# Performance work log

Measured on AMD Instinct MI355X. Metric: run time of the kernel, lower is better.

## Reference

```python
import jax, jax.numpy as jnp
import numpy as np

IN, HID, OUT = 128, 128, 128
NU, NI = 100000, 50000
E = 500000
NEG_SLOPE = 0.01  # torch F.leaky_relu default


def graph_conv(x_src, W, b, src, dst, n_dst):
    """DGL GraphConv with norm='right': sum messages into dst, divide by in-degree, add bias."""
    h = x_src @ W                                   # [n_src, d_out] -- apply weight first
    agg = jax.ops.segment_sum(h[src], dst, num_segments=n_dst)  # irregular gather + scatter-add
    deg = jax.ops.segment_sum(jnp.ones(dst.shape, h.dtype), dst, num_segments=n_dst)
    return agg / jnp.clip(deg, 1.0)[:, None] + b


def setup_inputs() -> dict:
    key = jax.random.key(0)
    ks = jax.random.split(key, 16)
    inp = {
        "x_user": jax.random.normal(ks[0], (NU, IN), jnp.float32),
        "x_item": jax.random.normal(ks[1], (NI, IN), jnp.float32),
        "src_rates": jax.random.randint(ks[2], (E,), 0, NU),
        "dst_rates": jax.random.randint(ks[3], (E,), 0, NI),
        "src_rev": jax.random.randint(ks[4], (E,), 0, NI),
        "dst_rev": jax.random.randint(ks[5], (E,), 0, NU),
        # layer 1 per-relation GraphConv params
        "W1_rates": jax.random.normal(ks[6], (IN, HID), jnp.float32) / np.sqrt(IN),
        "b1_rates": jnp.zeros((HID,), jnp.float32),
        "W1_rev": jax.random.normal(ks[7], (IN, HID), jnp.float32) / np.sqrt(IN),
        "b1_rev": jnp.zeros((HID,), jnp.float32),
        # layer 2 per-relation GraphConv params
        "W2_rates": jax.random.normal(ks[8], (HID, OUT), jnp.float32) / np.sqrt(HID),
        "b2_rates": jnp.zeros((OUT,), jnp.float32),
        "W2_rev": jax.random.normal(ks[9], (HID, OUT), jnp.float32) / np.sqrt(HID),
        "b2_rev": jnp.zeros((OUT,), jnp.float32),
    }
    return inp


def reference(x_user, x_item, src_rates, dst_rates, src_rev, dst_rev,
              W1_rates, b1_rates, W1_rev, b1_rev,
              W2_rates, b2_rates, W2_rev, b2_rev):
    # layer 1: HeteroGraphConv(sum) -- each dst type receives from its one incoming relation
    h_item = graph_conv(x_user, W1_rates, b1_rates, src_rates, dst_rates, NI)
    h_user = graph_conv(x_item, W1_rev, b1_rev, src_rev, dst_rev, NU)
    h_item = jax.nn.leaky_relu(h_item, NEG_SLOPE)
    h_user = jax.nn.leaky_relu(h_user, NEG_SLOPE)
    # layer 2
    o_item = graph_conv(h_user, W2_rates, b2_rates, src_rates, dst_rates, NI)
    o_user = graph_conv(h_item, W2_rev, b2_rev, src_rev, dst_rev, NU)
    return (o_user, o_item)
```

## Files before the change

### kernel.cpp

```cpp
#include <hip/hip_runtime.h>
#include <cstdint>
#include <cstddef>

#define NUSER 100000
#define NITEM 50000
#define NTOT  150000
#define NEDGE 500000
#define NEG_SLOPE 0.01f
#define PADW 136

#define BROWS 512
#define BSHIFT 9
#define NBUCK ((NTOT + BROWS - 1) / BROWS)
#define GCAP  8192
#define EPB   2048
#define NBINB ((NEDGE + EPB - 1) / EPB)
#define NENT  (2 * EPB)

typedef __attribute__((ext_vector_type(8))) short bf16x8;
typedef __attribute__((ext_vector_type(4))) float f32x4;

__device__ __forceinline__ unsigned short f2bf(float f) {
    unsigned int u = __builtin_bit_cast(unsigned int, f);
    unsigned int r = u + 0x7fffu + ((u >> 16) & 1u);
    return (unsigned short)(r >> 16);
}
__device__ __forceinline__ float bf2f(unsigned int b) {
    unsigned int u = (b & 0xffffu) << 16;
    return __builtin_bit_cast(float, u);
}
__device__ __forceinline__ unsigned int pack2(float lo, float hi) {
    return (unsigned int)f2bf(lo) | ((unsigned int)f2bf(hi) << 16);
}


__global__ __launch_bounds__(512) void bin_edges(const int* __restrict__ src_rates, const int* __restrict__ dst_rates,
                                                 const int* __restrict__ src_rev,   const int* __restrict__ dst_rev,
                                                 int* __restrict__ bcnt, unsigned int* __restrict__ bbuf) {
    __shared__ int h[NBUCK];
    __shared__ int hs[NBUCK];
    __shared__ int hbase[NBUCK];
    __shared__ int hcur[NBUCK];
    __shared__ int bsc[512];
    __shared__ unsigned int stage[NENT];

    int t = threadIdx.x;
    int e0 = blockIdx.x * EPB;
    int n = NEDGE - e0; if (n > EPB) n = EPB;

    for (int i = t; i < NBUCK; i += 512) h[i] = 0;
    __syncthreads();

    for (int i = t; i < n; i += 512) {
        int e = e0 + i;
        atomicAdd(&h[dst_rates[e] >> BSHIFT], 1);
        atomicAdd(&h[(NITEM + dst_rev[e]) >> BSHIFT], 1);
    }
    __syncthreads();

    int v = (t < NBUCK) ? h[t] : 0;
    bsc[t] = v;
    __syncthreads();
    for (int off = 1; off < 512; off <<= 1) {
        int x = (t >= off) ? bsc[t - off] : 0;
        __syncthreads();
        bsc[t] += x;
        __syncthreads();
    }
    if (t < NBUCK) {
        int run = bsc[t] - v;
        hs[t] = run;
        hcur[t] = run;
        hbase[t] = (v > 0) ? atomicAdd(&bcnt[t], v) : 0;
    }
    __syncthreads();

    for (int i = t; i < n; i += 512) {
        int e = e0 + i;
        int r1 = dst_rates[e];
        int p1 = atomicAdd(&hcur[r1 >> BSHIFT], 1);
        if (p1 < NENT)
            stage[p1] = ((unsigned)(r1 & (BROWS - 1)) << 17) | (unsigned)src_rates[e];
        int r2 = NITEM + dst_rev[e];
        int p2 = atomicAdd(&hcur[r2 >> BSHIFT], 1);
        if (p2 < NENT)
            stage[p2] = ((unsigned)(r2 & (BROWS - 1)) << 17) | (unsigned)src_rev[e];
    }
    __syncthreads();

    int wid = t >> 6, lane = t & 63;
    for (int b = wid; b < NBUCK; b += 8) {
        int cnt = h[b];
        if (cnt > NENT) cnt = NENT;
        int gb = hbase[b];
        int sb = hs[b];
        for (int i = lane; i < cnt; i += 64) {
            int gpos = gb + i;
            if (gpos < GCAP) bbuf[(size_t)b * GCAP + gpos] = stage[sb + i];
        }
    }
}


__global__ __launch_bounds__(256) void build_csr(const int* __restrict__ bcnt,
                                                 const unsigned int* __restrict__ bbuf,
                                                 int* __restrict__ rp, int* __restrict__ csr) {
    __shared__ unsigned int ent[GCAP];
    __shared__ int h[BROWS], hs[BROWS];
    __shared__ int bsc[256];

    int bk = blockIdx.x, t = threadIdx.x;

    int ps = 0;
    for (int i = t; i < bk; i += 256) ps += bcnt[i];
    bsc[t] = ps;
    __syncthreads();
    for (int off = 128; off > 0; off >>= 1) {
        if (t < off) bsc[t] += bsc[t + off];
        __syncthreads();
    }
    int base = bsc[0];
    int n = bcnt[bk];
    if (n > GCAP) n = GCAP;
    __syncthreads();

    const unsigned int* src = bbuf + (size_t)bk * GCAP;
    for (int i = t; i < n; i += 256) ent[i] = src[i];
    h[t] = 0; h[t + 256] = 0;
    __syncthreads();

    for (int i = t; i < n; i += 256) atomicAdd(&h[ent[i] >> 17], 1);
    __syncthreads();

    int v0 = h[2 * t], v1 = h[2 * t + 1];
    int ls = v0 + v1;
    bsc[t] = ls;
    __syncthreads();
    for (int off = 1; off < 256; off <<= 1) {
        int x = (t >= off) ? bsc[t - off] : 0;
        __syncthreads();
        bsc[t] += x;
        __syncthreads();
    }
    int run = bsc[t] - ls;
    hs[2 * t] = run;
    hs[2 * t + 1] = run + v0;
    __syncthreads();

    for (int r = t; r < BROWS; r += 256) {
        int row = bk * BROWS + r;
        if (row < NTOT) rp[row] = base + hs[r];
        h[r] = 0;
    }
    if (bk == 0 && t == 0) rp[NTOT] = 2 * NEDGE;
    __syncthreads();

    for (int i = t; i < n; i += 256) {
        unsigned int ev = ent[i];
        int rl = (int)(ev >> 17);
        int pos = base + hs[rl] + atomicAdd(&h[rl], 1);
        csr[pos] = (int)(ev & 0x1FFFFu);
    }
}


__global__ void wprep(const float* __restrict__ w0, const float* __restrict__ w1,
                      const float* __restrict__ w2, const float* __restrict__ w3,
                      unsigned short* __restrict__ wt) {
    const float* src = (blockIdx.x == 0) ? w0 : (blockIdx.x == 1) ? w1 : (blockIdx.x == 2) ? w2 : w3;
    unsigned short* dst = wt + (size_t)blockIdx.x * 128 * PADW;
    for (int i = threadIdx.x; i < 16384; i += 256) {
        int k = i >> 7, c = i & 127;
        dst[c * PADW + k] = f2bf(src[i]);
    }
}


__global__ __launch_bounds__(256) void aggregate_ep(const unsigned short* __restrict__ featA,
                                                    const unsigned short* __restrict__ featB,
                                                    const int* __restrict__ rp, const int* __restrict__ csr,
                                                    const float* __restrict__ bI, const float* __restrict__ bU,
                                                    unsigned short* __restrict__ outb,
                                                    float* __restrict__ outI, float* __restrict__ outU) {
    int row = blockIdx.x * 8 + (threadIdx.x >> 5);
    if (row >= NTOT) return;
    bool item = row < NITEM;
    const unsigned short* feat = item ? featA : featB;
    int l = threadIdx.x & 31;
    int sub = l >> 4, l16 = l & 15;
    int b = rp[row], e = rp[row + 1];
    float a0 = 0.f, a1 = 0.f, a2 = 0.f, a3 = 0.f, a4 = 0.f, a5 = 0.f, a6 = 0.f, a7 = 0.f;
    int j = b + sub;
    for (; j + 2 < e; j += 4) {
        int s0 = csr[j];
        int s1 = csr[j + 2];
        uint4 v0 = *((const uint4*)(feat + (size_t)s0 * 128) + l16);
        uint4 v1 = *((const uint4*)(feat + (size_t)s1 * 128) + l16);
        a0 += bf2f(v0.x); a1 += bf2f(v0.x >> 16);
        a2 += bf2f(v0.y); a3 += bf2f(v0.y >> 16);
        a4 += bf2f(v0.z); a5 += bf2f(v0.z >> 16);
        a6 += bf2f(v0.w); a7 += bf2f(v0.w >> 16);
        a0 += bf2f(v1.x); a1 += bf2f(v1.x >> 16);
        a2 += bf2f(v1.y); a3 += bf2f(v1.y >> 16);
        a4 += bf2f(v1.z); a5 += bf2f(v1.z >> 16);
        a6 += bf2f(v1.w); a7 += bf2f(v1.w >> 16);
    }
    if (j < e) {
        int s0 = csr[j];
        uint4 v0 = *((const uint4*)(feat + (size_t)s0 * 128) + l16);
        a0 += bf2f(v0.x); a1 += bf2f(v0.x >> 16);
        a2 += bf2f(v0.y); a3 += bf2f(v0.y >> 16);
        a4 += bf2f(v0.z); a5 += bf2f(v0.z >> 16);
        a6 += bf2f(v0.w); a7 += bf2f(v0.w >> 16);
    }
    a0 += __shfl_xor(a0, 16); a1 += __shfl_xor(a1, 16);
    a2 += __shfl_xor(a2, 16); a3 += __shfl_xor(a3, 16);
    a4 += __shfl_xor(a4, 16); a5 += __shfl_xor(a5, 16);
    a6 += __shfl_xor(a6, 16); a7 += __shfl_xor(a7, 16);
    if (sub == 0) {
        int deg = e - b;
        float inv = 1.0f / (float)(deg > 0 ? deg : 1);
        const float* bias = item ? bI : bU;
        float4 bv0 = ((const float4*)bias)[l16 * 2];
        float4 bv1 = ((const float4*)bias)[l16 * 2 + 1];
        float r0 = a0 * inv + bv0.x, r1 = a1 * inv + bv0.y;
        float r2 = a2 * inv + bv0.z, r3 = a3 * inv + bv0.w;
        float r4 = a4 * inv + bv1.x, r5 = a5 * inv + bv1.y;
        float r6 = a6 * inv + bv1.z, r7 = a7 * inv + bv1.w;
        if (outI) {
            float* o = item ? (outI + (size_t)row * 128) : (outU + (size_t)(row - NITEM) * 128);
            float4 o0, o1;
            o0.x = r0; o0.y = r1; o0.z = r2; o0.w = r3;
            o1.x = r4; o1.y = r5; o1.z = r6; o1.w = r7;
            ((float4*)o)[l16 * 2]     = o0;
            ((float4*)o)[l16 * 2 + 1] = o1;
        } else {
            r0 = r0 > 0.f ? r0 : NEG_SLOPE * r0;
            r1 = r1 > 0.f ? r1 : NEG_SLOPE * r1;
            r2 = r2 > 0.f ? r2 : NEG_SLOPE * r2;
            r3 = r3 > 0.f ? r3 : NEG_SLOPE * r3;
            r4 = r4 > 0.f ? r4 : NEG_SLOPE * r4;
            r5 = r5 > 0.f ? r5 : NEG_SLOPE * r5;
            r6 = r6 > 0.f ? r6 : NEG_SLOPE * r6;
            r7 = r7 > 0.f ? r7 : NEG_SLOPE * r7;
            uint4 o;
            o.x = pack2(r0, r1);
            o.y = pack2(r2, r3);
            o.z = pack2(r4, r5);
            o.w = pack2(r6, r7);
            *((uint4*)(outb + (size_t)row * 128) + l16) = o;
        }
    }
}


__global__ __launch_bounds__(256) void gemm_both(const float* __restrict__ xfU, const float* __restrict__ xfI,
                                                 const unsigned short* __restrict__ inB,
                                                 const unsigned short* __restrict__ wt0,
                                                 const unsigned short* __restrict__ wt1,
                                                 unsigned short* __restrict__ outB,
                                                 int nR0, int g0, int g1) {
    __shared__ __attribute__((aligned(16))) unsigned short wl[128 * PADW];
    __shared__ __attribute__((aligned(16))) unsigned short xl[64 * PADW];
    int t = threadIdx.x;
    int bi = blockIdx.x;
    bool reg0 = bi < g0;
    int tbeg = reg0 ? bi : bi - g0;
    int gstr = reg0 ? g0 : g1;
    int rbeg = reg0 ? 0 : nR0;
    int rcnt = reg0 ? nR0 : NTOT - nR0;
    int Nend = rbeg + rcnt;
    int nT = (rcnt + 63) / 64;
    const unsigned short* wt = reg0 ? wt0 : wt1;

    for (int i = t; i < 128 * PADW / 8; i += 256)
        ((uint4*)wl)[i] = ((const uint4*)wt)[i];

    int lane = t & 63, w = t >> 6;
    int l16 = lane & 15, kq = lane >> 4;
    int rowb = w * 16;

    for (int tt = tbeg; tt < nT; tt += gstr) {
        int row0 = rbeg + tt * 64;

        __syncthreads();
        if (xfU) {
            for (int i = t; i < 1024; i += 256) {
                int r = i >> 4, c = i & 15;
                int row = row0 + r;
                uint4 v = make_uint4(0u, 0u, 0u, 0u);
                if (row < Nend) {
                    const float* s = (row < NUSER) ? (xfU + (size_t)row * 128 + c * 8)
                                                   : (xfI + (size_t)(row - NUSER) * 128 + c * 8);
                    float4 a = ((const float4*)s)[0];
                    float4 b = ((const float4*)s)[1];
                    v.x = pack2(a.x, a.y);
                    v.y = pack2(a.z, a.w);
                    v.z = pack2(b.x, b.y);
                    v.w = pack2(b.z, b.w);
                }
                ((uint4*)xl)[r * (PADW / 8) + c] = v;
            }
        } else {
            for (int i = t; i < 1024; i += 256) {
                int r = i >> 4, c = i & 15;
                int row = row0 + r;
                uint4 v = make_uint4(0u, 0u, 0u, 0u);
                if (row < Nend) v = ((const uint4*)(inB + (size_t)row * 128))[c];
                ((uint4*)xl)[r * (PADW / 8) + c] = v;
            }
        }
        __syncthreads();

        f32x4 acc[8];
        #pragma unroll
        for (int i = 0; i < 8; ++i) acc[i] = (f32x4){0.f, 0.f, 0.f, 0.f};

        #pragma unroll
        for (int ks = 0; ks < 4; ++ks) {
            int ko = ks * 32 + kq * 8;
            bf16x8 af = *(const bf16x8*)&xl[(rowb + l16) * PADW + ko];
            #pragma unroll
            for (int t8 = 0; t8 < 8; ++t8) {
                bf16x8 bf = *(const bf16x8*)&wl[(t8 * 16 + l16) * PADW + ko];
                acc[t8] = __builtin_amdgcn_mfma_f32_16x16x32_bf16(af, bf, acc[t8], 0, 0, 0);
            }
        }

        #pragma unroll
        for (int t8 = 0; t8 < 8; ++t8) {
            #pragma unroll
            for (int j = 0; j < 4; ++j)
                xl[(rowb + kq * 4 + j) * PADW + t8 * 16 + l16] = f2bf(acc[t8][j]);
        }
        __syncthreads();
        for (int i = t; i < 1024; i += 256) {
            int r = i >> 4, c = i & 15;
            int row = row0 + r;
            if (row < Nend)
                ((uint4*)(outB + (size_t)row * 128))[c] = ((uint4*)xl)[r * (PADW / 8) + c];
        }
    }
}


extern "C" void kernel_launch(void* const* d_in, const int* in_sizes, int n_in,
                              void* d_out, int out_size, void* d_ws, size_t ws_size,
                              hipStream_t stream) {
    const float* x_user    = (const float*)d_in[0];
    const float* x_item    = (const float*)d_in[1];
    const int*   src_rates = (const int*)d_in[2];
    const int*   dst_rates = (const int*)d_in[3];
    const int*   src_rev   = (const int*)d_in[4];
    const int*   dst_rev   = (const int*)d_in[5];
    const float* W1_rates  = (const float*)d_in[6];
    const float* b1_rates  = (const float*)d_in[7];
    const float* W1_rev    = (const float*)d_in[8];
    const float* b1_rev    = (const float*)d_in[9];
    const float* W2_rates  = (const float*)d_in[10];
    const float* b2_rates  = (const float*)d_in[11];
    const float* W2_rev    = (const float*)d_in[12];
    const float* b2_rev    = (const float*)d_in[13];

    float* out    = (float*)d_out;
    float* o_user = out;
    float* o_item = out + (size_t)NUSER * 128;

    char* ws = (char*)d_ws;
    size_t off = 0;
    auto carve = [&](size_t bytes) -> void* {
        void* p = ws + off;
        off = (off + bytes + 255) & ~(size_t)255;
        return p;
    };
    unsigned short* A = (unsigned short*)carve((size_t)NTOT * 128 * 2);
    unsigned short* B = (unsigned short*)carve((size_t)NTOT * 128 * 2);
    int* rp    = (int*)carve((size_t)(NTOT + 1) * 4);
    int* bcnt  = (int*)carve((size_t)NBUCK * 4);
    int* csr   = (int*)carve((size_t)(2 * NEDGE) * 4);
    unsigned short* wtAll = (unsigned short*)carve((size_t)4 * 128 * PADW * 2);
    unsigned short* Wt1_rates = wtAll;
    unsigned short* Wt1_rev   = wtAll + 1 * (size_t)128 * PADW;
    unsigned short* Wt2_rates = wtAll + 2 * (size_t)128 * PADW;
    unsigned short* Wt2_rev   = wtAll + 3 * (size_t)128 * PADW;

    unsigned int* bbuf = (unsigned int*)B;

    hipMemsetAsync(bcnt, 0, (size_t)NBUCK * 4, stream);
    wprep<<<4, 256, 0, stream>>>(W1_rates, W1_rev, W2_rates, W2_rev, wtAll);
    bin_edges<<<NBINB, 512, 0, stream>>>(src_rates, dst_rates, src_rev, dst_rev, bcnt, bbuf);
    build_csr<<<NBUCK, 256, 0, stream>>>(bcnt, bbuf, rp, csr);

    int nbAgg = (NTOT + 7) / 8;

    gemm_both<<<528, 256, 0, stream>>>(x_user, x_item, nullptr,
                                       Wt1_rates, Wt1_rev, A, NUSER, 352, 176);
    aggregate_ep<<<nbAgg, 256, 0, stream>>>(A, A + (size_t)NUSER * 128, rp, csr,
                                            b1_rates, b1_rev, B, nullptr, nullptr);

    gemm_both<<<528, 256, 0, stream>>>(nullptr, nullptr, B,
                                       Wt2_rev, Wt2_rates, A, NITEM, 176, 352);
    aggregate_ep<<<nbAgg, 256, 0, stream>>>(A + (size_t)NITEM * 128, A, rp, csr,
                                            b2_rates, b2_rev, nullptr, o_item, o_user);
}
```

Before: 201.3 us.

## Fuse weight prep into edge binning and CSR build into first GEMM

Weight transposition/bf16 conversion now runs as extra blocks of the edge-binning kernel, and the CSR construction blocks share a launch with the layer-1 GEMM blocks through a shared-memory union. Both pairs are independent, so this removes two kernel launches and lets the work overlap on the GPU instead of running back to back. The fused kernel uses the larger of the two shared-memory footprints for every block, which may reduce occupancy. Block scheduling order may also leave one part of the work running late.

```diff
diff --git a/kernel.cpp b/kernel.cpp
--- a/kernel.cpp
+++ b/kernel.cpp
@@ -17,6 +17,10 @@
 #define NBINB ((NEDGE + EPB - 1) / EPB)
 #define NENT  (2 * EPB)
 
+#define GB_U 352
+#define GB_I 176
+#define GB1  (GB_U + GB_I)
+
 typedef __attribute__((ext_vector_type(8))) short bf16x8;
 typedef __attribute__((ext_vector_type(4))) float f32x4;
 
@@ -34,9 +38,23 @@
 }
 
 
-__global__ __launch_bounds__(512) void bin_edges(const int* __restrict__ src_rates, const int* __restrict__ dst_rates,
+__global__ __launch_bounds__(512) void bin_wprep(const int* __restrict__ src_rates, const int* __restrict__ dst_rates,
                                                  const int* __restrict__ src_rev,   const int* __restrict__ dst_rev,
-                                                 int* __restrict__ bcnt, unsigned int* __restrict__ bbuf) {
+                                                 int* __restrict__ bcnt, unsigned int* __restrict__ bbuf,
+                                                 const float* __restrict__ w0, const float* __restrict__ w1,
+                                                 const float* __restrict__ w2, const float* __restrict__ w3,
+                                                 unsigned short* __restrict__ wt) {
+    if (blockIdx.x >= NBINB) {
+        int widx = blockIdx.x - NBINB;
+        const float* src = (widx == 0) ? w0 : (widx == 1) ? w1 : (widx == 2) ? w2 : w3;
+        unsigned short* dst = wt + (size_t)widx * 128 * PADW;
+        for (int i = threadIdx.x; i < 16384; i += 512) {
+            int k = i >> 7, c = i & 127;
+            dst[c * PADW + k] = f2bf(src[i]);
+        }
+        return;
+    }
+
     __shared__ int h[NBUCK];
     __shared__ int hs[NBUCK];
     __shared__ int hbase[NBUCK];
@@ -102,14 +120,99 @@
 }
 
 
-__global__ __launch_bounds__(256) void build_csr(const int* __restrict__ bcnt,
+struct GemmSm { unsigned short wl[128 * PADW]; unsigned short xl[64 * PADW]; };
+struct CsrSm  { unsigned int ent[GCAP]; int h[BROWS]; int hs[BROWS]; int bsc[256]; };
+union FusedSm { GemmSm g; CsrSm c; };
+
+__global__ __launch_bounds__(256) void csr_gemm1(const int* __restrict__ bcnt,
                                                  const unsigned int* __restrict__ bbuf,
-                                                 int* __restrict__ rp, int* __restrict__ csr) {
-    __shared__ unsigned int ent[GCAP];
-    __shared__ int h[BROWS], hs[BROWS];
-    __shared__ int bsc[256];
-
-    int bk = blockIdx.x, t = threadIdx.x;
+                                                 int* __restrict__ rp, int* __restrict__ csr,
+                                                 const float* __restrict__ xfU, const float* __restrict__ xfI,
+                                                 const unsigned short* __restrict__ wt0,
+                                                 const unsigned short* __restrict__ wt1,
+                                                 unsigned short* __restrict__ outB) {
+    __shared__ __attribute__((aligned(16))) FusedSm sm;
+    int t = threadIdx.x;
+    int bi = blockIdx.x;
+
+    if (bi < GB1) {
+        unsigned short* wl = sm.g.wl;
+        unsigned short* xl = sm.g.xl;
+        bool reg0 = bi < GB_U;
+        int tbeg = reg0 ? bi : bi - GB_U;
+        int gstr = reg0 ? GB_U : GB_I;
+        int rbeg = reg0 ? 0 : NUSER;
+        int rcnt = reg0 ? NUSER : NITEM;
+        int Nend = rbeg + rcnt;
+        int nT = (rcnt + 63) / 64;
+        const unsigned short* wt = reg0 ? wt0 : wt1;
+
+        for (int i = t; i < 128 * PADW / 8; i += 256)
+            ((uint4*)wl)[i] = ((const uint4*)wt)[i];
+
+        int lane = t & 63, w = t >> 6;
+        int l16 = lane & 15, kq = lane >> 4;
+        int rowb = w * 16;
+
+        for (int tt = tbeg; tt < nT; tt += gstr) {
+            int row0 = rbeg + tt * 64;
+
+            __syncthreads();
+            for (int i = t; i < 1024; i += 256) {
+                int r = i >> 4, c = i & 15;
+                int row = row0 + r;
+                uint4 v = make_uint4(0u, 0u, 0u, 0u);
+                if (row < Nend) {
+                    const float* s = (row < NUSER) ? (xfU + (size_t)row * 128 + c * 8)
+                                                   : (xfI + (size_t)(row - NUSER) * 128 + c * 8);
+                    float4 a = ((const float4*)s)[0];
+                    float4 b = ((const float4*)s)[1];
+                    v.x = pack2(a.x, a.y);
+                    v.y = pack2(a.z, a.w);
+                    v.z = pack2(b.x, b.y);
+                    v.w = pack2(b.z, b.w);
+                }
+                ((uint4*)xl)[r * (PADW / 8) + c] = v;
+            }
+            __syncthreads();
+
+            f32x4 acc[8];
+            #pragma unroll
+            for (int i = 0; i < 8; ++i) acc[i] = (f32x4){0.f, 0.f, 0.f, 0.f};
+
+            #pragma unroll
+            for (int ks = 0; ks < 4; ++ks) {
+                int ko = ks * 32 + kq * 8;
+                bf16x8 af = *(const bf16x8*)&xl[(rowb + l16) * PADW + ko];
+                #pragma unroll
+                for (int t8 = 0; t8 < 8; ++t8) {
+                    bf16x8 bf = *(const bf16x8*)&wl[(t8 * 16 + l16) * PADW + ko];
+                    acc[t8] = __builtin_amdgcn_mfma_f32_16x16x32_bf16(af, bf, acc[t8], 0, 0, 0);
+                }
+            }
+
+            #pragma unroll
+            for (int t8 = 0; t8 < 8; ++t8) {
+                #pragma unroll
+                for (int j = 0; j < 4; ++j)
+                    xl[(rowb + kq * 4 + j) * PADW + t8 * 16 + l16] = f2bf(acc[t8][j]);
+            }
+            __syncthreads();
+            for (int i = t; i < 1024; i += 256) {
+                int r = i >> 4, c = i & 15;
+                int row = row0 + r;
+                if (row < Nend)
+                    ((uint4*)(outB + (size_t)row * 128))[c] = ((uint4*)xl)[r * (PADW / 8) + c];
+            }
+        }
+        return;
+    }
+
+    unsigned int* ent = sm.c.ent;
+    int* h  = sm.c.h;
+    int* hsx = sm.c.hs;
+    int* bsc = sm.c.bsc;
+    int bk = bi - GB1;
 
     int ps = 0;
     for (int i = t; i < bk; i += 256) ps += bcnt[i];
@@ -143,13 +246,13 @@
         __syncthreads();
     }
     int run = bsc[t] - ls;
-    hs[2 * t] = run;
-    hs[2 * t + 1] = run + v0;
+    hsx[2 * t] = run;
+    hsx[2 * t + 1] = run + v0;
     __syncthreads();
 
     for (int r = t; r < BROWS; r += 256) {
         int row = bk * BROWS + r;
-        if (row < NTOT) rp[row] = base + hs[r];
+        if (row < NTOT) rp[row] = base + hsx[r];
         h[r] = 0;
     }
     if (bk == 0 && t == 0) rp[NTOT] = 2 * NEDGE;
@@ -158,20 +261,8 @@
     for (int i = t; i < n; i += 256) {
         unsigned int ev = ent[i];
         int rl = (int)(ev >> 17);
-        int pos = base + hs[rl] + atomicAdd(&h[rl], 1);
+        int pos = base + hsx[rl] + atomicAdd(&h[rl], 1);
         csr[pos] = (int)(ev & 0x1FFFFu);
-    }
-}
-
-
-__global__ void wprep(const float* __restrict__ w0, const float* __restrict__ w1,
-                      const float* __restrict__ w2, const float* __restrict__ w3,
-                      unsigned short* __restrict__ wt) {
-    const float* src = (blockIdx.x == 0) ? w0 : (blockIdx.x == 1) ? w1 : (blockIdx.x == 2) ? w2 : w3;
-    unsigned short* dst = wt + (size_t)blockIdx.x * 128 * PADW;
-    for (int i = threadIdx.x; i < 16384; i += 256) {
-        int k = i >> 7, c = i & 127;
-        dst[c * PADW + k] = f2bf(src[i]);
     }
 }
 
@@ -254,8 +345,7 @@
 }
 
 
-__global__ __launch_bounds__(256) void gemm_both(const float* __restrict__ xfU, const float* __restrict__ xfI,
-                                                 const unsigned short* __restrict__ inB,
+__global__ __launch_bounds__(256) void gemm_both(const unsigned short* __restrict__ inB,
                                                  const unsigned short* __restrict__ wt0,
                                                  const unsigned short* __restrict__ wt1,
                                                  unsigned short* __restrict__ outB,
@@ -284,31 +374,12 @@
         int row0 = rbeg + tt * 64;
 
         __syncthreads();
-        if (xfU) {
-            for (int i = t; i < 1024; i += 256) {
-                int r = i >> 4, c = i & 15;
-                int row = row0 + r;
-                uint4 v = make_uint4(0u, 0u, 0u, 0u);
-                if (row < Nend) {
-                    const float* s = (row < NUSER) ? (xfU + (size_t)row * 128 + c * 8)
-                                                   : (xfI + (size_t)(row - NUSER) * 128 + c * 8);
-                    float4 a = ((const float4*)s)[0];
-                    float4 b = ((const float4*)s)[1];
-                    v.x = pack2(a.x, a.y);
-                    v.y = pack2(a.z, a.w);
-                    v.z = pack2(b.x, b.y);
-                    v.w = pack2(b.z, b.w);
-                }
-                ((uint4*)xl)[r * (PADW / 8) + c] = v;
-            }
-        } else {
-            for (int i = t; i < 1024; i += 256) {
-                int r = i >> 4, c = i & 15;
-                int row = row0 + r;
-                uint4 v = make_uint4(0u, 0u, 0u, 0u);
-                if (row < Nend) v = ((const uint4*)(inB + (size_t)row * 128))[c];
-                ((uint4*)xl)[r * (PADW / 8) + c] = v;
-            }
+        for (int i = t; i < 1024; i += 256) {
+            int r = i >> 4, c = i & 15;
+            int row = row0 + r;
+            uint4 v = make_uint4(0u, 0u, 0u, 0u);
+            if (row < Nend) v = ((const uint4*)(inB + (size_t)row * 128))[c];
+            ((uint4*)xl)[r * (PADW / 8) + c] = v;
         }
         __syncthreads();
 
@@ -387,19 +458,19 @@
     unsigned int* bbuf = (unsigned int*)B;
 
     hipMemsetAsync(bcnt, 0, (size_t)NBUCK * 4, stream);
-    wprep<<<4, 256, 0, stream>>>(W1_rates, W1_rev, W2_rates, W2_rev, wtAll);
-    bin_edges<<<NBINB, 512, 0, stream>>>(src_rates, dst_rates, src_rev, dst_rev, bcnt, bbuf);
-    build_csr<<<NBUCK, 256, 0, stream>>>(bcnt, bbuf, rp, csr);
+    bin_wprep<<<NBINB + 4, 512, 0, stream>>>(src_rates, dst_rates, src_rev, dst_rev, bcnt, bbuf,
+                                             W1_rates, W1_rev, W2_rates, W2_rev, wtAll);
+
+    csr_gemm1<<<GB1 + NBUCK, 256, 0, stream>>>(bcnt, bbuf, rp, csr,
+                                               x_user, x_item, Wt1_rates, Wt1_rev, A);
 
     int nbAgg = (NTOT + 7) / 8;
 
-    gemm_both<<<528, 256, 0, stream>>>(x_user, x_item, nullptr,
-                                       Wt1_rates, Wt1_rev, A, NUSER, 352, 176);
     aggregate_ep<<<nbAgg, 256, 0, stream>>>(A, A + (size_t)NUSER * 128, rp, csr,
                                             b1_rates, b1_rev, B, nullptr, nullptr);
 
-    gemm_both<<<528, 256, 0, stream>>>(nullptr, nullptr, B,
-                                       Wt2_rev, Wt2_rates, A, NITEM, 176, 352);
+    gemm_both<<<528, 256, 0, stream>>>(B, Wt2_rev, Wt2_rates, A, NITEM, 176, 352);
+
     aggregate_ep<<<nbAgg, 256, 0, stream>>>(A + (size_t)NITEM * 128, A, rp, csr,
                                             b2_rates, b2_rev, nullptr, o_item, o_user);
 }
```

Result: faster. 173.1 us, median of 3 (-14.0%).
